# Optimization experiments

Hardware: AMD Instinct MI355X
Metric: run time of the kernel (lower is better)

## Reference

```python
import jax, jax.numpy as jnp
import numpy as np
import math

B, N, D = 8, 4096, 256
Q = 0.5
K = 8  # max_order
EPS = 1e-5


def scale_norm(x, g):
    n = jnp.linalg.norm(x, axis=-1, keepdims=True)
    return g * x / jnp.maximum(n, EPS)


def siren(x, w1, b1, g, w2, b2):
    # nn.Linear uses y = x @ W.T + b with W [out, in]
    h = jnp.sin(jnp.einsum('bnd,ed->bne', x, w1) + b1)
    h = scale_norm(h, g)
    return jnp.sin(jnp.einsum('bnd,ed->bne', h, w2) + b2)


def adaptive_avg_pool6(x):
    # AdaptiveAvgPool1d(6) over last dim (torch semantics: bin j = mean(x[floor(jL/6):ceil((j+1)L/6)]))
    L = x.shape[-1]
    cols = []
    for j in range(6):
        s = (j * L) // 6
        e = -((-(j + 1) * L) // 6)
        cols.append(jnp.mean(x[..., s:e], axis=-1))
    return jnp.stack(cols, axis=-1)


def jackson_damp(k_max):
    c = math.pi / (k_max + 2)
    k = np.arange(k_max + 1)
    d = ((k_max + 2 - k) * math.sin(c) * np.cos(k * c) + math.cos(c) * np.sin(k * c)) / ((k_max + 2) * math.sin(c))
    d[0] = 1.0
    return jnp.asarray(d, dtype=jnp.float32)


def cheb_gibbs(seq, coef, damp):
    # seq [B,N], coef [B,K+1], damp [K+1] (rows of module buffer are identical)
    out = coef[:, 0:1] + seq * coef[:, 1:2] * damp[1]
    tx0, tx1 = jnp.ones_like(seq), seq
    for k in range(2, K + 1):
        tx2 = 2.0 * seq * tx1 - tx0
        out = out + tx2 * coef[:, k:k + 1] * damp[k]
        tx0, tx1 = tx1, tx2
    return out


def givens(alpha, beta, gamma):
    ra = (alpha + beta) * (math.pi / 2.0)
    rs = (alpha - beta) * (math.pi / 2.0)
    gm = gamma * (math.pi / 2.0)
    cg, sg = jnp.cos(gm), jnp.sin(gm)
    g_ii = jnp.exp(-1j * ra) * cg
    g_ij = jnp.exp(-1j * rs) * sg
    g_ji = -jnp.exp(1j * rs) * sg
    g_jj = jnp.exp(1j * ra) * cg
    return g_ii, g_ij, g_ji, g_jj


def dhhp(x, li, lij, lji, ljj, ui, uij, uji, ujj, diag_pre=None, diag_post=None):
    # x [B,N,D] complex; Givens factors [B,N-1]. Banded Hessenberg transform Z = G_l (G_u x).
    if diag_pre is not None:
        x = diag_pre[:, :, None] * x
    y0 = ui[:, 0:1, None] * x[:, 0:1] + uij[:, 0:1, None] * x[:, 1:2]
    ym = (uji[:, :-1, None] * x[:, :-2]
          + (ujj[:, :-1] * ui[:, 1:])[:, :, None] * x[:, 1:-1]
          + (ujj[:, :-1] * uij[:, 1:])[:, :, None] * x[:, 2:])
    yl = uji[:, -1:, None] * x[:, -2:-1] + ujj[:, -1:, None] * x[:, -1:]
    Y = jnp.concatenate([y0, ym, yl], axis=1)
    z0 = li[:, 0:1, None] * Y[:, 0:1] + lij[:, 0:1, None] * Y[:, 1:2]
    zm = ((li[:, 1:] * lji[:, :-1])[:, :, None] * Y[:, :-2]
          + (li[:, 1:] * ljj[:, :-1])[:, :, None] * Y[:, 1:-1]
          + lij[:, 1:, None] * Y[:, 2:])
    zl = lji[:, -1:, None] * Y[:, -2:-1] + ljj[:, -1:, None] * Y[:, -1:]
    Z = jnp.concatenate([z0, zm, zl], axis=1)
    if diag_post is not None:
        Z = diag_post[:, :, None] * Z
    return Z


def chsyconv(x, ev_w1, ev_b1, ev_g, ev_w2, ev_b2, hp_w1, hp_b1, hp_g, hp_w2, hp_b2, cheb_coef):
    # eigenvalue hypernetwork: mean over feat dim (pool_dim=2) -> [B,N]
    eig = jnp.mean(siren(x, ev_w1, ev_b1, ev_g, ev_w2, ev_b2), axis=2)
    filt = cheb_gibbs(eig, cheb_coef, jackson_damp(K))  # KPM-filtered eigenvalues
    diag = filt.astype(jnp.complex64) * jnp.exp(2j * math.pi * Q * eig)  # magnetic complex diagonal
    # eigenvector hyperparameters: pool feat->6, view [B,6N], chunk into 6 along dim 1
    pooled = adaptive_avg_pool6(siren(x, hp_w1, hp_b1, hp_g, hp_w2, hp_b2)).reshape(B, 6 * N)
    a_l, b_l, g_l, a_u, b_u, g_u = jnp.split(pooled, 6, axis=1)
    l_ii, l_ij, l_ji, l_jj = givens(a_l[:, 1:], b_l[:, 1:], g_l[:, 1:])
    u_ii, u_ij, u_ji, u_jj = givens(a_u[:, :-1], b_u[:, :-1], g_u[:, :-1])
    xc = x.astype(jnp.complex64)
    # DHHP transform (transform=True): diagonal filter applied after the banded transform
    Z = dhhp(xc, l_ii, l_ij, l_ji, l_jj, u_ii, u_ij, u_ji, u_jj, diag_post=diag)
    # inverse DHHP: conjugate-transpose Givens factors (ii<->jj, ij->-ij, ji->-ji), no diagonal
    out = dhhp(Z, l_jj, -l_ij, -l_ji, l_ii, u_jj, -u_ij, -u_ji, u_ii)
    return out  # complex64 [B,N,D] (value dropout is identity in eval)


def setup_inputs():
    key = jax.random.key(0)
    ks = jax.random.split(key, 5)
    bound = math.sqrt(6.0 / D)
    x = jax.random.normal(ks[0], (B, N, D), dtype=jnp.float32)
    ev_w1 = jax.random.uniform(ks[1], (D, D), jnp.float32, -bound, bound)
    ev_w2 = jax.random.uniform(ks[2], (D, D), jnp.float32, -bound, bound)
    hp_w1 = jax.random.uniform(ks[3], (D, D), jnp.float32, -bound, bound)
    hp_w2 = jax.random.uniform(ks[4], (D, D), jnp.float32, -bound, bound)
    zb = jnp.zeros((D,), jnp.float32)
    g = jnp.asarray(math.sqrt(D), jnp.float32)  # ScaleNorm scale init
    cheb_coef = jnp.full((B, K + 1), 2.0 / (K + 1), jnp.float32).at[:, 0].set(1.0 / (K + 1))
    return {"x": x, "ev_w1": ev_w1, "ev_b1": zb, "ev_g": g, "ev_w2": ev_w2, "ev_b2": zb,
            "hp_w1": hp_w1, "hp_b1": zb, "hp_g": g, "hp_w2": hp_w2, "hp_b2": zb,
            "cheb_coef": cheb_coef}


def reference(x, ev_w1, ev_b1, ev_g, ev_w2, ev_b2, hp_w1, hp_b1, hp_g, hp_w2, hp_b2, cheb_coef):
    return chsyconv(x, ev_w1, ev_b1, ev_g, ev_w2, ev_b2, hp_w1, hp_b1, hp_g, hp_w2, hp_b2, cheb_coef)
```

## Files before the change

kernel.cpp:

```cpp
#include <hip/hip_runtime.h>
#include <math.h>

typedef __attribute__((ext_vector_type(8))) _Float16 f16x8;
typedef __attribute__((ext_vector_type(4))) float    f32x4;

static constexpr int cB  = 8;
static constexpr int cN  = 4096;
static constexpr int cD  = 256;
static constexpr int cBN = cB * cN;
#define PI_F 3.14159265358979323846f

__device__ __forceinline__ float2 cmul(float2 a, float2 b) {
    return make_float2(a.x*b.x - a.y*b.y, a.x*b.y + a.y*b.x);
}
__device__ __forceinline__ float2 cfma2(float2 a, float2 b, float2 acc) {
    acc.x += a.x*b.x - a.y*b.y;
    acc.y += a.x*b.y + a.y*b.x;
    return acc;
}
__device__ __forceinline__ float2 cneg(float2 a) { return make_float2(-a.x, -a.y); }

struct G4 { float2 ii, ij, ji, jj; };

__device__ __forceinline__ G4 givens_f(float al, float be, float ga) {
    float ra = (al + be) * (PI_F * 0.5f);
    float rs = (al - be) * (PI_F * 0.5f);
    float gm = ga * (PI_F * 0.5f);
    float sg, cg, sra, cra, srs, crs;
    sincosf(gm, &sg, &cg);
    sincosf(ra, &sra, &cra);
    sincosf(rs, &srs, &crs);
    G4 g;
    g.ii = make_float2( cra*cg, -sra*cg);
    g.ij = make_float2( crs*sg, -srs*sg);
    g.ji = make_float2(-crs*sg, -srs*sg);
    g.jj = make_float2( cra*cg,  sra*cg);
    return g;
}

__global__ void sentinel_kernel(float* out, int n, float v) {
    if (n > 0) out[0] = v;
    if (n > 1) out[1] = v;
}

__global__ __launch_bounds__(256) void wcvt_kernel(
    const float* __restrict__ w0, const float* __restrict__ w1,
    const float* __restrict__ w2, const float* __restrict__ w3,
    _Float16* __restrict__ W16)
{
    int i = blockIdx.x * 256 + threadIdx.x;
    const float* src[4] = {w0, w1, w2, w3};
    #pragma unroll
    for (int m = 0; m < 4; ++m)
        W16[(size_t)m*65536 + i] = (_Float16)src[m][i];
}

__device__ __forceinline__ void stage_x16(const float* __restrict__ xrow0,
                                          _Float16* buf, int tid)
{
    const int row = tid >> 3;
    const int c0  = (tid & 7) * 32;
    const float4* src = (const float4*)(xrow0 + row*256 + c0);
    const int swz = (row & 7) << 4;
    #pragma unroll
    for (int j = 0; j < 4; ++j) {
        float4 p = src[2*j], q = src[2*j+1];
        f16x8 h;
        h[0]=(_Float16)p.x; h[1]=(_Float16)p.y; h[2]=(_Float16)p.z; h[3]=(_Float16)p.w;
        h[4]=(_Float16)q.x; h[5]=(_Float16)q.y; h[6]=(_Float16)q.z; h[7]=(_Float16)q.w;
        int off = (((c0 + j*8) * 2) ^ swz);
        *(f16x8*)((char*)buf + row*512 + off) = h;
    }
}

__device__ __forceinline__ void ld_a1(const _Float16* src, int k0, int lr, int kq,
                                      f16x8 ah[4])
{
    #pragma unroll
    for (int mt = 0; mt < 4; ++mt) {
        int row = mt*16 + lr;
        int off = ((k0*2 + kq*16) ^ ((row & 7) << 4));
        ah[mt] = *(const f16x8*)((const char*)src + row*512 + off);
    }
}

__device__ __forceinline__ void ld_w1(const _Float16* __restrict__ wP,
                                      int k0, int w, int lr, int kq, f16x8 bh[2])
{
    #pragma unroll
    for (int nt = 0; nt < 2; ++nt) {
        int col = w*32 + nt*16 + lr;
        bh[nt] = *(const f16x8*)(wP + col*256 + k0 + kq*8);
    }
}

__device__ __forceinline__ void do_mfma8(const f16x8 ah[4], const f16x8 bh[2],
                                         f32x4 acc[4][2])
{
    #pragma unroll
    for (int mt = 0; mt < 4; ++mt)
        #pragma unroll
        for (int nt = 0; nt < 2; ++nt)
            acc[mt][nt] = __builtin_amdgcn_mfma_f32_16x16x32_f16(ah[mt], bh[nt], acc[mt][nt], 0, 0, 0);
}

__device__ __forceinline__ void gemm32(const _Float16* aSrc,
                                       const _Float16* __restrict__ wP,
                                       int w, int lr, int kq, f32x4 acc[4][2])
{
    f16x8 ah[4];
    f16x8 b0[2], b1[2];
    ld_w1(wP, 0, w, lr, kq, b0);
    #pragma unroll
    for (int kk = 0; kk < 8; ++kk) {
        ld_a1(aSrc, kk*32, lr, kq, ah);
        if ((kk & 1) == 0) {
            if (kk < 7) ld_w1(wP, (kk+1)*32, w, lr, kq, b1);
            do_mfma8(ah, b0, acc);
        } else {
            if (kk < 7) ld_w1(wP, (kk+1)*32, w, lr, kq, b0);
            do_mfma8(ah, b1, acc);
        }
    }
}

__global__ __launch_bounds__(512, 2) void siren_mfma(
    const float* __restrict__ x, const _Float16* __restrict__ W16,
    const float* __restrict__ ev_b1, const float* __restrict__ ev_g,
    const float* __restrict__ ev_b2,
    const float* __restrict__ hp_b1, const float* __restrict__ hp_g,
    const float* __restrict__ hp_b2,
    const float* __restrict__ cheb,
    float* __restrict__ Pout, float2* __restrict__ DIAG)
{
    __shared__ _Float16 buf[64*256];
    __shared__ float red[8][64];

    const int tid  = threadIdx.x;
    const int w    = tid >> 6;
    const int lane = tid & 63;
    const int lr   = lane & 15;
    const int kq   = lane >> 4;
    const size_t r0 = (size_t)blockIdx.x * 64;
    const int b   = (int)(r0 >> 12);
    const int net = blockIdx.y;

    const _Float16* w1P = W16 + (size_t)(net*2 + 0)*65536;
    const _Float16* w2P = W16 + (size_t)(net*2 + 1)*65536;
    const float* b1 = net ? hp_b1 : ev_b1;
    const float* b2 = net ? hp_b2 : ev_b2;
    const float  g  = net ? hp_g[0] : ev_g[0];

    stage_x16(x + r0*256, buf, tid);
    __syncthreads();

    f32x4 acc[4][2];
    #pragma unroll
    for (int mt = 0; mt < 4; ++mt)
        #pragma unroll
        for (int nt = 0; nt < 2; ++nt) acc[mt][nt] = (f32x4)(0.f);
    gemm32(buf, w1P, w, lr, kq, acc);

    {
        float bv[2] = { b1[w*32 + lr], b1[w*32 + 16 + lr] };
        float rn[4][4];
        #pragma unroll
        for (int mt = 0; mt < 4; ++mt)
            #pragma unroll
            for (int r = 0; r < 4; ++r) {
                float s = 0.f;
                #pragma unroll
                for (int nt = 0; nt < 2; ++nt) {
                    float v = __sinf(acc[mt][nt][r] + bv[nt]);
                    s += v*v;
                }
                rn[mt][r] = s;
            }
        #pragma unroll
        for (int mk = 1; mk < 16; mk <<= 1)
            #pragma unroll
            for (int mt = 0; mt < 4; ++mt)
                #pragma unroll
                for (int r = 0; r < 4; ++r) rn[mt][r] += __shfl_xor(rn[mt][r], mk);
        if (lr == 0)
            #pragma unroll
            for (int mt = 0; mt < 4; ++mt)
                #pragma unroll
                for (int r = 0; r < 4; ++r) red[w][mt*16 + kq*4 + r] = rn[mt][r];
        __syncthreads();
        #pragma unroll
        for (int mt = 0; mt < 4; ++mt)
            #pragma unroll
            for (int r = 0; r < 4; ++r) {
                int row = mt*16 + kq*4 + r;
                float tot = 0.f;
                #pragma unroll
                for (int ww = 0; ww < 8; ++ww) tot += red[ww][row];
                float sc = g / fmaxf(sqrtf(tot), 1e-5f);
                int swz = (row & 7) << 4;
                #pragma unroll
                for (int nt = 0; nt < 2; ++nt) {
                    float v = __sinf(acc[mt][nt][r] + bv[nt]) * sc;
                    int col = w*32 + nt*16 + lr;
                    *(_Float16*)((char*)buf + row*512 + ((col*2) ^ swz)) = (_Float16)v;
                }
            }
    }
    __syncthreads();

    #pragma unroll
    for (int mt = 0; mt < 4; ++mt)
        #pragma unroll
        for (int nt = 0; nt < 2; ++nt) acc[mt][nt] = (f32x4)(0.f);
    gemm32(buf, w2P, w, lr, kq, acc);

    if (net == 0) {
        float bv[2] = { b2[w*32 + lr], b2[w*32 + 16 + lr] };
        float es[4][4];
        #pragma unroll
        for (int mt = 0; mt < 4; ++mt)
            #pragma unroll
            for (int r = 0; r < 4; ++r) {
                float s = 0.f;
                #pragma unroll
                for (int nt = 0; nt < 2; ++nt) s += __sinf(acc[mt][nt][r] + bv[nt]);
                es[mt][r] = s;
            }
        #pragma unroll
        for (int mk = 1; mk < 16; mk <<= 1)
            #pragma unroll
            for (int mt = 0; mt < 4; ++mt)
                #pragma unroll
                for (int r = 0; r < 4; ++r) es[mt][r] += __shfl_xor(es[mt][r], mk);
        if (lr == 0)
            #pragma unroll
            for (int mt = 0; mt < 4; ++mt)
                #pragma unroll
                for (int r = 0; r < 4; ++r) red[w][mt*16 + kq*4 + r] = es[mt][r];
        __syncthreads();
        if (tid < 64) {
            int row = tid;
            float tot = 0.f;
            #pragma unroll
            for (int ww = 0; ww < 8; ++ww) tot += red[ww][row];
            float ev = tot * (1.f/256.f);
            float dmp[9];
            {
                const double c = 3.14159265358979323846 / 10.0;
                double sc = sin(c), cc = cos(c);
                dmp[0] = 1.f;
                for (int k = 1; k < 9; ++k)
                    dmp[k] = (float)(((10.0 - k) * sc * cos(k*c) + cc * sin(k*c)) / (10.0 * sc));
            }
            const float* cf = cheb + b*9;
            float t0 = 1.f, t1 = ev;
            float filt = cf[0] + ev * cf[1] * dmp[1];
            #pragma unroll
            for (int k = 2; k < 9; ++k) {
                float t2 = 2.f*ev*t1 - t0;
                filt += t2 * cf[k] * dmp[k];
                t0 = t1; t1 = t2;
            }
            float sp, cp;
            sincosf(PI_F * ev, &sp, &cp);
            DIAG[r0 + row] = make_float2(filt*cp, filt*sp);
        }
    } else {
        __syncthreads();
        float bv[2] = { b2[w*32 + lr], b2[w*32 + 16 + lr] };
        #pragma unroll
        for (int mt = 0; mt < 4; ++mt)
            #pragma unroll
            for (int r = 0; r < 4; ++r) {
                int row = mt*16 + kq*4 + r;
                int swz = (row & 7) << 4;
                #pragma unroll
                for (int nt = 0; nt < 2; ++nt) {
                    float v = __sinf(acc[mt][nt][r] + bv[nt]);
                    int col = w*32 + nt*16 + lr;
                    *(_Float16*)((char*)buf + row*512 + ((col*2) ^ swz)) = (_Float16)v;
                }
            }
        __syncthreads();
        if (tid < 384) {
            const int sb[6] = {0, 42, 85, 128, 170, 213};
            const int eb[6] = {43, 86, 128, 171, 214, 256};
            const float inv[6] = {1.f/43.f, 1.f/44.f, 1.f/43.f, 1.f/43.f, 1.f/44.f, 1.f/43.f};
            int row = tid / 6, q = tid - row*6;
            int swz = (row & 7) << 4;
            float s = 0.f;
            for (int c = sb[q]; c < eb[q]; ++c)
                s += (float)(*(const _Float16*)((const char*)buf + row*512 + ((c*2) ^ swz)));
            int nn = (int)(r0 & 4095) + row;
            Pout[(size_t)b*6*cN + nn*6 + q] = s * inv[q];
        }
    }
}

__global__ __launch_bounds__(256) void dhhp_stencil(
    const float* __restrict__ x, const float* __restrict__ P,
    const float2* __restrict__ DIAG, float* __restrict__ outf,
    unsigned long long out_floats, int mode)
{
    __shared__ float  xsr[40*256];
    __shared__ G4 uG[41], lG[41];
    __shared__ float2 cDg[40];
    __shared__ float2 cT[32][9];

    const int tid = threadIdx.x;
    const int n0 = blockIdx.x * 32;
    const int b  = blockIdx.y;
    const size_t bbase = (size_t)b * cN;
    const int b6 = b * 6 * cN;
    const float2 z2 = make_float2(0.f, 0.f);
    const int jb = n0 - 5;

    for (int idx = tid; idx < 40*64; idx += 256) {
        int r = idx >> 6, d4 = idx & 63;
        int m = n0 - 4 + r;
        float4 v = make_float4(0.f, 0.f, 0.f, 0.f);
        if (m >= 0 && m < cN) v = *(const float4*)(x + (bbase + m)*cD + d4*4);
        *(float4*)(xsr + r*256 + d4*4) = v;
    }
    if (tid < 82) {
        int t = (tid < 41) ? tid : tid - 41;
        int j = jb + t;
        G4 g; g.ii = g.ij = g.ji = g.jj = z2;
        if (j >= 0 && j <= cN-2) {
            if (tid < 41) g = givens_f(P[b6+3*cN+j], P[b6+4*cN+j], P[b6+5*cN+j]);
            else          g = givens_f(P[b6+j+1],    P[b6+cN+j+1], P[b6+2*cN+j+1]);
        }
        if (tid < 41) uG[t] = g; else lG[t] = g;
    } else if (tid < 122) {
        int t = tid - 82;
        int m = n0 - 4 + t;
        cDg[t] = (m >= 0 && m < cN) ? DIAG[bbase + m] : z2;
    }
    __syncthreads();

    if (tid < 32) {
        const int m = n0 + tid;
        auto scoef = [&](int s, int rr, float2& A, float2& B, float2& C) {
            A = z2; B = z2; C = z2;
            if (rr < 0 || rr >= cN) return;
            if (s == 1) {
                if (rr == 0)         { G4 u0 = uG[0-jb]; B = u0.ii; C = u0.ij; }
                else if (rr == cN-1) { G4 up = uG[rr-1-jb]; A = up.ji; B = up.jj; }
                else { G4 up = uG[rr-1-jb], uc = uG[rr-jb];
                       A = up.ji; B = cmul(up.jj, uc.ii); C = cmul(up.jj, uc.ij); }
            } else if (s == 2) {
                if (rr == 0)         { G4 l0 = lG[0-jb]; B = l0.ii; C = l0.ij; }
                else if (rr == cN-1) { G4 lp = lG[rr-1-jb]; A = lp.ji; B = lp.jj; }
                else { G4 lp = lG[rr-1-jb], lc = lG[rr-jb];
                       A = cmul(lc.ii, lp.ji); B = cmul(lc.ii, lp.jj); C = lc.ij; }
            } else if (s == 3) {
                if (rr == 0)         { G4 u0 = uG[0-jb]; B = u0.jj; C = cneg(u0.ij); }
                else if (rr == cN-1) { G4 up = uG[rr-1-jb]; A = cneg(up.ji); B = up.ii; }
                else { G4 up = uG[rr-1-jb], uc = uG[rr-jb];
                       A = cneg(up.ji); B = cmul(up.ii, uc.jj); C = cneg(cmul(up.ii, uc.ij)); }
            } else {
                if (rr == 0)         { G4 l0 = lG[0-jb]; B = l0.jj; C = cneg(l0.ij); }
                else if (rr == cN-1) { G4 lp = lG[rr-1-jb]; A = cneg(lp.ji); B = lp.ii; }
                else { G4 lp = lG[rr-1-jb], lc = lG[rr-jb];
                       A = cneg(cmul(lc.jj, lp.ji)); B = cmul(lc.jj, lp.ii); C = cneg(lc.ij); }
            }
        };

        float2 wv[9], nw[9];
        #pragma unroll
        for (int k = 0; k < 9; ++k) wv[k] = z2;
        {
            float2 A, B, C; scoef(4, m, A, B, C);
            wv[3] = A; wv[4] = B; wv[5] = C;
        }
        #pragma unroll
        for (int k = 0; k < 9; ++k) nw[k] = z2;
        #pragma unroll
        for (int i = 3; i <= 5; ++i) {
            float2 A, B, C; scoef(3, m + i - 4, A, B, C);
            nw[i-1] = cfma2(wv[i], A, nw[i-1]);
            nw[i]   = cfma2(wv[i], B, nw[i]);
            nw[i+1] = cfma2(wv[i], C, nw[i+1]);
        }
        #pragma unroll
        for (int k = 0; k < 9; ++k) wv[k] = nw[k];
        #pragma unroll
        for (int k = 2; k <= 6; ++k) wv[k] = cmul(wv[k], cDg[tid + k]);
        #pragma unroll
        for (int k = 0; k < 9; ++k) nw[k] = z2;
        #pragma unroll
        for (int i = 2; i <= 6; ++i) {
            float2 A, B, C; scoef(2, m + i - 4, A, B, C);
            nw[i-1] = cfma2(wv[i], A, nw[i-1]);
            nw[i]   = cfma2(wv[i], B, nw[i]);
            nw[i+1] = cfma2(wv[i], C, nw[i+1]);
        }
        #pragma unroll
        for (int k = 0; k < 9; ++k) wv[k] = nw[k];
        #pragma unroll
        for (int k = 0; k < 9; ++k) nw[k] = z2;
        #pragma unroll
        for (int i = 1; i <= 7; ++i) {
            float2 A, B, C; scoef(1, m + i - 4, A, B, C);
            nw[i-1] = cfma2(wv[i], A, nw[i-1]);
            nw[i]   = cfma2(wv[i], B, nw[i]);
            nw[i+1] = cfma2(wv[i], C, nw[i+1]);
        }
        #pragma unroll
        for (int k = 0; k < 9; ++k) cT[tid][k] = nw[k];
    }
    __syncthreads();

    for (int idx = tid; idx < 32*64; idx += 256) {
        int r = idx >> 6, d4 = idx & 63;
        float4 ox = make_float4(0.f, 0.f, 0.f, 0.f);
        float4 oy = make_float4(0.f, 0.f, 0.f, 0.f);
        #pragma unroll
        for (int j = 0; j < 9; ++j) {
            float4 xv = *(const float4*)(xsr + (r + j)*256 + d4*4);
            float2 t = cT[r][j];
            ox.x = fmaf(t.x, xv.x, ox.x); ox.y = fmaf(t.x, xv.y, ox.y);
            ox.z = fmaf(t.x, xv.z, ox.z); ox.w = fmaf(t.x, xv.w, ox.w);
            oy.x = fmaf(t.y, xv.x, oy.x); oy.y = fmaf(t.y, xv.y, oy.y);
            oy.z = fmaf(t.y, xv.z, oy.z); oy.w = fmaf(t.y, xv.w, oy.w);
        }
        unsigned long long ci = (unsigned long long)((bbase + n0 + r)*(size_t)cD + d4*4);
        if (mode == 0) {
            if (ci + 4ULL <= out_floats) *(float4*)(outf + ci) = ox;
        } else {
            if (2ULL*(ci + 4ULL) <= out_floats) {
                float2* o2 = (float2*)outf + ci;
                o2[0] = make_float2(ox.x, oy.x);
                o2[1] = make_float2(ox.y, oy.y);
                o2[2] = make_float2(ox.z, oy.z);
                o2[3] = make_float2(ox.w, oy.w);
            }
        }
    }
}

extern "C" void kernel_launch(void* const* d_in, const int* in_sizes, int n_in,
                              void* d_out, int out_size, void* d_ws, size_t ws_size,
                              hipStream_t stream)
{
    const int expect[12] = { cBN*cD, cD*cD, cD, 1, cD*cD, cD,
                             cD*cD, cD, 1, cD*cD, cD, cB*9 };
    bool ok = (n_in == 12);
    if (ok) for (int i = 0; i < 12; ++i) ok = ok && (in_sizes[i] == expect[i]);
    if (!ok) {
        sentinel_kernel<<<1, 1, 0, stream>>>((float*)d_out, out_size, 1.0e6f);
        return;
    }
    const size_t pBytes = (size_t)cB * 6 * cN * sizeof(float);
    const size_t dBytes = (size_t)cBN * sizeof(float2);
    const size_t wBytes = (size_t)4 * 65536 * sizeof(_Float16);
    if (d_ws == nullptr || ws_size < pBytes + dBytes + wBytes) {
        sentinel_kernel<<<1, 1, 0, stream>>>((float*)d_out, out_size, 2.0e6f);
        return;
    }
    int mode;
    if (out_size == cBN * cD)          mode = 0;
    else if (out_size == 2 * cBN * cD) mode = 1;
    else {
        sentinel_kernel<<<1, 1, 0, stream>>>((float*)d_out, out_size, 3.0e6f);
        return;
    }

    const float* x     = (const float*)d_in[0];
    const float* ev_w1 = (const float*)d_in[1];
    const float* ev_b1 = (const float*)d_in[2];
    const float* ev_g  = (const float*)d_in[3];
    const float* ev_w2 = (const float*)d_in[4];
    const float* ev_b2 = (const float*)d_in[5];
    const float* hp_w1 = (const float*)d_in[6];
    const float* hp_b1 = (const float*)d_in[7];
    const float* hp_g  = (const float*)d_in[8];
    const float* hp_w2 = (const float*)d_in[9];
    const float* hp_b2 = (const float*)d_in[10];
    const float* cheb  = (const float*)d_in[11];

    float*     P    = (float*)d_ws;
    float2*    DIAG = (float2*)((char*)d_ws + pBytes);
    _Float16*  W16  = (_Float16*)((char*)d_ws + pBytes + dBytes);

    wcvt_kernel<<<dim3(256), 256, 0, stream>>>(ev_w1, ev_w2, hp_w1, hp_w2, W16);
    siren_mfma<<<dim3(cBN/64, 2), 512, 0, stream>>>(x, W16, ev_b1, ev_g, ev_b2,
                                                    hp_b1, hp_g, hp_b2, cheb, P, DIAG);
    dhhp_stencil<<<dim3(cN/32, cB), 256, 0, stream>>>(x, P, DIAG, (float*)d_out,
                                                      (unsigned long long)out_size,
                                                      mode);
}
```

Baseline: 83.61 us.

## Give each wave full rows in siren MFMA to drop cross-wave reductions

The SIREN GEMM tiling moves from each wave owning a 32-column slice of a 64-row tile to each wave owning 16 full rows of a 128-row tile. Row norms and row means then reduce inside a wave with shuffles, so the shared reduction array and most block-wide barriers go away; those barriers become per-wave LDS waits. Each wave now streams all 256 weight columns from global memory per k-step and holds 16 accumulator tiles, which raises register pressure and weight traffic per wave. The grid shrinks by half in exchange.

```diff
diff --git a/kernel.cpp b/kernel.cpp
--- a/kernel.cpp
+++ b/kernel.cpp
@@ -55,71 +55,41 @@
         W16[(size_t)m*65536 + i] = (_Float16)src[m][i];
 }
 
-__device__ __forceinline__ void stage_x16(const float* __restrict__ xrow0,
-                                          _Float16* buf, int tid)
-{
-    const int row = tid >> 3;
-    const int c0  = (tid & 7) * 32;
-    const float4* src = (const float4*)(xrow0 + row*256 + c0);
-    const int swz = (row & 7) << 4;
-    #pragma unroll
-    for (int j = 0; j < 4; ++j) {
-        float4 p = src[2*j], q = src[2*j+1];
-        f16x8 h;
-        h[0]=(_Float16)p.x; h[1]=(_Float16)p.y; h[2]=(_Float16)p.z; h[3]=(_Float16)p.w;
-        h[4]=(_Float16)q.x; h[5]=(_Float16)q.y; h[6]=(_Float16)q.z; h[7]=(_Float16)q.w;
-        int off = (((c0 + j*8) * 2) ^ swz);
-        *(f16x8*)((char*)buf + row*512 + off) = h;
-    }
-}
-
-__device__ __forceinline__ void ld_a1(const _Float16* src, int k0, int lr, int kq,
-                                      f16x8 ah[4])
-{
-    #pragma unroll
-    for (int mt = 0; mt < 4; ++mt) {
-        int row = mt*16 + lr;
-        int off = ((k0*2 + kq*16) ^ ((row & 7) << 4));
-        ah[mt] = *(const f16x8*)((const char*)src + row*512 + off);
-    }
-}
-
-__device__ __forceinline__ void ld_w1(const _Float16* __restrict__ wP,
-                                      int k0, int w, int lr, int kq, f16x8 bh[2])
-{
-    #pragma unroll
-    for (int nt = 0; nt < 2; ++nt) {
-        int col = w*32 + nt*16 + lr;
-        bh[nt] = *(const f16x8*)(wP + col*256 + k0 + kq*8);
-    }
-}
-
-__device__ __forceinline__ void do_mfma8(const f16x8 ah[4], const f16x8 bh[2],
-                                         f32x4 acc[4][2])
-{
-    #pragma unroll
-    for (int mt = 0; mt < 4; ++mt)
-        #pragma unroll
-        for (int nt = 0; nt < 2; ++nt)
-            acc[mt][nt] = __builtin_amdgcn_mfma_f32_16x16x32_f16(ah[mt], bh[nt], acc[mt][nt], 0, 0, 0);
-}
-
-__device__ __forceinline__ void gemm32(const _Float16* aSrc,
-                                       const _Float16* __restrict__ wP,
-                                       int w, int lr, int kq, f32x4 acc[4][2])
-{
-    f16x8 ah[4];
-    f16x8 b0[2], b1[2];
-    ld_w1(wP, 0, w, lr, kq, b0);
+__device__ __forceinline__ void wave_wait_lds() {
+    asm volatile("s_waitcnt lgkmcnt(0)" ::: "memory");
+    __builtin_amdgcn_sched_barrier(0);
+}
+
+__device__ __forceinline__ f16x8 ld_a(const _Float16* buf, int row, int k0, int kq)
+{
+    int off = ((k0*2 + kq*16) ^ ((row & 7) << 4));
+    return *(const f16x8*)((const char*)buf + row*512 + off);
+}
+
+__device__ __forceinline__ f16x8 ld_w(const _Float16* __restrict__ wP,
+                                      int nt, int kk, int lr, int kq)
+{
+    return *(const f16x8*)(wP + (nt*16 + lr)*256 + kk*32 + kq*8);
+}
+
+__device__ __forceinline__ void gemmR(const _Float16* buf,
+                                      const _Float16* __restrict__ wP,
+                                      int wrow, int lr, int kq, f32x4 acc[16])
+{
     #pragma unroll
     for (int kk = 0; kk < 8; ++kk) {
-        ld_a1(aSrc, kk*32, lr, kq, ah);
-        if ((kk & 1) == 0) {
-            if (kk < 7) ld_w1(wP, (kk+1)*32, w, lr, kq, b1);
-            do_mfma8(ah, b0, acc);
-        } else {
-            if (kk < 7) ld_w1(wP, (kk+1)*32, w, lr, kq, b0);
-            do_mfma8(ah, b1, acc);
+        f16x8 ah = ld_a(buf, wrow + lr, kk*32, kq);
+        f16x8 b0 = ld_w(wP, 0, kk, lr, kq);
+        f16x8 b1;
+        #pragma unroll
+        for (int nt = 0; nt < 16; ++nt) {
+            if ((nt & 1) == 0) {
+                if (nt < 15) b1 = ld_w(wP, nt+1, kk, lr, kq);
+                acc[nt] = __builtin_amdgcn_mfma_f32_16x16x32_f16(ah, b0, acc[nt], 0, 0, 0);
+            } else {
+                if (nt < 15) b0 = ld_w(wP, nt+1, kk, lr, kq);
+                acc[nt] = __builtin_amdgcn_mfma_f32_16x16x32_f16(ah, b1, acc[nt], 0, 0, 0);
+            }
         }
     }
 }
@@ -133,15 +103,15 @@
     const float* __restrict__ cheb,
     float* __restrict__ Pout, float2* __restrict__ DIAG)
 {
-    __shared__ _Float16 buf[64*256];
-    __shared__ float red[8][64];
+    __shared__ _Float16 buf[128*256];
 
     const int tid  = threadIdx.x;
     const int w    = tid >> 6;
     const int lane = tid & 63;
     const int lr   = lane & 15;
     const int kq   = lane >> 4;
-    const size_t r0 = (size_t)blockIdx.x * 64;
+    const int wrow = w * 16;
+    const size_t r0 = (size_t)blockIdx.x * 128;
     const int b   = (int)(r0 >> 12);
     const int net = blockIdx.y;
 
@@ -151,142 +121,122 @@
     const float* b2 = net ? hp_b2 : ev_b2;
     const float  g  = net ? hp_g[0] : ev_g[0];
 
-    stage_x16(x + r0*256, buf, tid);
+    {
+        const int row = tid >> 2;
+        const int c0  = (tid & 3) * 64;
+        const float4* src = (const float4*)(x + (r0 + row)*256 + c0);
+        const int swz = (row & 7) << 4;
+        #pragma unroll
+        for (int j = 0; j < 8; ++j) {
+            float4 p = src[2*j], q = src[2*j+1];
+            f16x8 h;
+            h[0]=(_Float16)p.x; h[1]=(_Float16)p.y; h[2]=(_Float16)p.z; h[3]=(_Float16)p.w;
+            h[4]=(_Float16)q.x; h[5]=(_Float16)q.y; h[6]=(_Float16)q.z; h[7]=(_Float16)q.w;
+            int off = (((c0 + j*8) * 2) ^ swz);
+            *(f16x8*)((char*)buf + row*512 + off) = h;
+        }
+    }
     __syncthreads();
 
-    f32x4 acc[4][2];
+    f32x4 acc[16];
     #pragma unroll
-    for (int mt = 0; mt < 4; ++mt)
-        #pragma unroll
-        for (int nt = 0; nt < 2; ++nt) acc[mt][nt] = (f32x4)(0.f);
-    gemm32(buf, w1P, w, lr, kq, acc);
+    for (int nt = 0; nt < 16; ++nt) acc[nt] = (f32x4)(0.f);
+    gemmR(buf, w1P, wrow, lr, kq, acc);
 
     {
-        float bv[2] = { b1[w*32 + lr], b1[w*32 + 16 + lr] };
-        float rn[4][4];
-        #pragma unroll
-        for (int mt = 0; mt < 4; ++mt)
+        float rs[4] = {0.f, 0.f, 0.f, 0.f};
+        #pragma unroll
+        for (int nt = 0; nt < 16; ++nt) {
+            float bv = b1[nt*16 + lr];
             #pragma unroll
             for (int r = 0; r < 4; ++r) {
-                float s = 0.f;
+                float v = __sinf(acc[nt][r] + bv);
+                rs[r] += v*v;
+            }
+        }
+        #pragma unroll
+        for (int mk = 1; mk < 16; mk <<= 1)
+            #pragma unroll
+            for (int r = 0; r < 4; ++r) rs[r] += __shfl_xor(rs[r], mk);
+        float sc[4];
+        #pragma unroll
+        for (int r = 0; r < 4; ++r) sc[r] = g / fmaxf(sqrtf(rs[r]), 1e-5f);
+        #pragma unroll
+        for (int nt = 0; nt < 16; ++nt) {
+            float bv = b1[nt*16 + lr];
+            #pragma unroll
+            for (int r = 0; r < 4; ++r) {
+                float v = __sinf(acc[nt][r] + bv) * sc[r];
+                int row = wrow + kq*4 + r;
+                int col = nt*16 + lr;
+                *(_Float16*)((char*)buf + row*512 + ((col*2) ^ ((row & 7) << 4))) = (_Float16)v;
+            }
+        }
+    }
+    wave_wait_lds();
+
+    #pragma unroll
+    for (int nt = 0; nt < 16; ++nt) acc[nt] = (f32x4)(0.f);
+    gemmR(buf, w2P, wrow, lr, kq, acc);
+
+    if (net == 0) {
+        float es[4] = {0.f, 0.f, 0.f, 0.f};
+        #pragma unroll
+        for (int nt = 0; nt < 16; ++nt) {
+            float bv = b2[nt*16 + lr];
+            #pragma unroll
+            for (int r = 0; r < 4; ++r) es[r] += __sinf(acc[nt][r] + bv);
+        }
+        #pragma unroll
+        for (int mk = 1; mk < 16; mk <<= 1)
+            #pragma unroll
+            for (int r = 0; r < 4; ++r) es[r] += __shfl_xor(es[r], mk);
+        float dmp[9];
+        {
+            const double c = 3.14159265358979323846 / 10.0;
+            double sc_ = sin(c), cc = cos(c);
+            dmp[0] = 1.f;
+            #pragma unroll
+            for (int k = 1; k < 9; ++k)
+                dmp[k] = (float)(((10.0 - k) * sc_ * cos(k*c) + cc * sin(k*c)) / (10.0 * sc_));
+        }
+        const float* cf = cheb + b*9;
+        #pragma unroll
+        for (int r = 0; r < 4; ++r) {
+            if (lr == r) {
+                float ev = es[r] * (1.f/256.f);
+                float t0 = 1.f, t1 = ev;
+                float filt = cf[0] + ev * cf[1] * dmp[1];
                 #pragma unroll
-                for (int nt = 0; nt < 2; ++nt) {
-                    float v = __sinf(acc[mt][nt][r] + bv[nt]);
-                    s += v*v;
+                for (int k = 2; k < 9; ++k) {
+                    float t2 = 2.f*ev*t1 - t0;
+                    filt += t2 * cf[k] * dmp[k];
+                    t0 = t1; t1 = t2;
                 }
-                rn[mt][r] = s;
-            }
-        #pragma unroll
-        for (int mk = 1; mk < 16; mk <<= 1)
-            #pragma unroll
-            for (int mt = 0; mt < 4; ++mt)
-                #pragma unroll
-                for (int r = 0; r < 4; ++r) rn[mt][r] += __shfl_xor(rn[mt][r], mk);
-        if (lr == 0)
-            #pragma unroll
-            for (int mt = 0; mt < 4; ++mt)
-                #pragma unroll
-                for (int r = 0; r < 4; ++r) red[w][mt*16 + kq*4 + r] = rn[mt][r];
-        __syncthreads();
-        #pragma unroll
-        for (int mt = 0; mt < 4; ++mt)
+                float sp, cp;
+                sincosf(PI_F * ev, &sp, &cp);
+                DIAG[r0 + wrow + kq*4 + r] = make_float2(filt*cp, filt*sp);
+            }
+        }
+    } else {
+        #pragma unroll
+        for (int nt = 0; nt < 16; ++nt) {
+            float bv = b2[nt*16 + lr];
             #pragma unroll
             for (int r = 0; r < 4; ++r) {
-                int row = mt*16 + kq*4 + r;
-                float tot = 0.f;
-                #pragma unroll
-                for (int ww = 0; ww < 8; ++ww) tot += red[ww][row];
-                float sc = g / fmaxf(sqrtf(tot), 1e-5f);
-                int swz = (row & 7) << 4;
-                #pragma unroll
-                for (int nt = 0; nt < 2; ++nt) {
-                    float v = __sinf(acc[mt][nt][r] + bv[nt]) * sc;
-                    int col = w*32 + nt*16 + lr;
-                    *(_Float16*)((char*)buf + row*512 + ((col*2) ^ swz)) = (_Float16)v;
-                }
-            }
-    }
-    __syncthreads();
-
-    #pragma unroll
-    for (int mt = 0; mt < 4; ++mt)
-        #pragma unroll
-        for (int nt = 0; nt < 2; ++nt) acc[mt][nt] = (f32x4)(0.f);
-    gemm32(buf, w2P, w, lr, kq, acc);
-
-    if (net == 0) {
-        float bv[2] = { b2[w*32 + lr], b2[w*32 + 16 + lr] };
-        float es[4][4];
-        #pragma unroll
-        for (int mt = 0; mt < 4; ++mt)
-            #pragma unroll
-            for (int r = 0; r < 4; ++r) {
-                float s = 0.f;
-                #pragma unroll
-                for (int nt = 0; nt < 2; ++nt) s += __sinf(acc[mt][nt][r] + bv[nt]);
-                es[mt][r] = s;
-            }
-        #pragma unroll
-        for (int mk = 1; mk < 16; mk <<= 1)
-            #pragma unroll
-            for (int mt = 0; mt < 4; ++mt)
-                #pragma unroll
-                for (int r = 0; r < 4; ++r) es[mt][r] += __shfl_xor(es[mt][r], mk);
-        if (lr == 0)
-            #pragma unroll
-            for (int mt = 0; mt < 4; ++mt)
-                #pragma unroll
-                for (int r = 0; r < 4; ++r) red[w][mt*16 + kq*4 + r] = es[mt][r];
-        __syncthreads();
-        if (tid < 64) {
-            int row = tid;
-            float tot = 0.f;
-            #pragma unroll
-            for (int ww = 0; ww < 8; ++ww) tot += red[ww][row];
-            float ev = tot * (1.f/256.f);
-            float dmp[9];
-            {
-                const double c = 3.14159265358979323846 / 10.0;
-                double sc = sin(c), cc = cos(c);
-                dmp[0] = 1.f;
-                for (int k = 1; k < 9; ++k)
-                    dmp[k] = (float)(((10.0 - k) * sc * cos(k*c) + cc * sin(k*c)) / (10.0 * sc));
-            }
-            const float* cf = cheb + b*9;
-            float t0 = 1.f, t1 = ev;
-            float filt = cf[0] + ev * cf[1] * dmp[1];
-            #pragma unroll
-            for (int k = 2; k < 9; ++k) {
-                float t2 = 2.f*ev*t1 - t0;
-                filt += t2 * cf[k] * dmp[k];
-                t0 = t1; t1 = t2;
-            }
-            float sp, cp;
-            sincosf(PI_F * ev, &sp, &cp);
-            DIAG[r0 + row] = make_float2(filt*cp, filt*sp);
-        }
-    } else {
-        __syncthreads();
-        float bv[2] = { b2[w*32 + lr], b2[w*32 + 16 + lr] };
-        #pragma unroll
-        for (int mt = 0; mt < 4; ++mt)
-            #pragma unroll
-            for (int r = 0; r < 4; ++r) {
-                int row = mt*16 + kq*4 + r;
-                int swz = (row & 7) << 4;
-                #pragma unroll
-                for (int nt = 0; nt < 2; ++nt) {
-                    float v = __sinf(acc[mt][nt][r] + bv[nt]);
-                    int col = w*32 + nt*16 + lr;
-                    *(_Float16*)((char*)buf + row*512 + ((col*2) ^ swz)) = (_Float16)v;
-                }
-            }
-        __syncthreads();
-        if (tid < 384) {
-            const int sb[6] = {0, 42, 85, 128, 170, 213};
-            const int eb[6] = {43, 86, 128, 171, 214, 256};
-            const float inv[6] = {1.f/43.f, 1.f/44.f, 1.f/43.f, 1.f/43.f, 1.f/44.f, 1.f/43.f};
-            int row = tid / 6, q = tid - row*6;
+                float v = __sinf(acc[nt][r] + bv);
+                int row = wrow + kq*4 + r;
+                int col = nt*16 + lr;
+                *(_Float16*)((char*)buf + row*512 + ((col*2) ^ ((row & 7) << 4))) = (_Float16)v;
+            }
+        }
+        wave_wait_lds();
+        const int sb[6] = {0, 42, 85, 128, 170, 213};
+        const int eb[6] = {43, 86, 128, 171, 214, 256};
+        const float inv[6] = {1.f/43.f, 1.f/44.f, 1.f/43.f, 1.f/43.f, 1.f/44.f, 1.f/43.f};
+        for (int t = lane; t < 96; t += 64) {
+            int rr = t / 6, q = t - rr*6;
+            int row = wrow + rr;
             int swz = (row & 7) << 4;
             float s = 0.f;
             for (int c = sb[q]; c < eb[q]; ++c)
@@ -484,8 +434,8 @@
     _Float16*  W16  = (_Float16*)((char*)d_ws + pBytes + dBytes);
 
     wcvt_kernel<<<dim3(256), 256, 0, stream>>>(ev_w1, ev_w2, hp_w1, hp_w2, W16);
-    siren_mfma<<<dim3(cBN/64, 2), 512, 0, stream>>>(x, W16, ev_b1, ev_g, ev_b2,
-                                                    hp_b1, hp_g, hp_b2, cheb, P, DIAG);
+    siren_mfma<<<dim3(cBN/128, 2), 512, 0, stream>>>(x, W16, ev_b1, ev_g, ev_b2,
+                                                     hp_b1, hp_g, hp_b2, cheb, P, DIAG);
     dhhp_stencil<<<dim3(cN/32, cB), 256, 0, stream>>>(x, P, DIAG, (float*)d_out,
                                                       (unsigned long long)out_size,
                                                       mode);
```

Result: slower. 175.2 us (+109.5%).
